# Kernel tuning notes

Hardware: AMD Instinct MI355X
Metric: run time of the kernel (lower is better)

Reference implementation:

```python
import jax, jax.numpy as jnp
import numpy as np

B, LQ, LK, DQ, DK, DV, H = 8, 256, 1024, 512, 512, 512, 128
NEG = -1000000.0

def setup_inputs() -> dict:
    key = jax.random.key(0)
    kq, kk, kv, kl, kwq, kwk, kwv = jax.random.split(key, 7)
    return {
        "Q": jax.random.normal(kq, (B, LQ, DQ), dtype=jnp.float32),
        "K": jax.random.normal(kk, (B, LK, DK), dtype=jnp.float32),
        "V": jax.random.normal(kv, (B, LK, DV), dtype=jnp.float32),
        "valid_lengths": jax.random.randint(kl, (B,), 1, LK + 1),
        "W_q": jax.random.normal(kwq, (DQ, H), dtype=jnp.float32) / np.sqrt(DQ),
        "W_k": jax.random.normal(kwk, (DK, H), dtype=jnp.float32) / np.sqrt(DK),
        "w_v": jax.random.normal(kwv, (H,), dtype=jnp.float32) / np.sqrt(H),
    }

def reference(Q, K, V, valid_lengths, W_q, W_k, w_v):
    # Projections
    q = Q @ W_q                      # (B, LQ, H)
    k = K @ W_k                      # (B, LK, H)
    # Additive (Bahdanau) features: broadcast add + tanh
    feat = jnp.tanh(q[:, :, None, :] + k[:, None, :, :])  # (B, LQ, LK, H)
    scores = jnp.einsum('bqkh,h->bqk', feat, w_v)          # (B, LQ, LK)
    # Masked softmax over keys (valid_lengths broadcast over all queries)
    mask = jnp.arange(LK)[None, None, :] < valid_lengths[:, None, None]
    scores = jnp.where(mask, scores, NEG)
    attn = jax.nn.softmax(scores, axis=-1)                 # (B, LQ, LK)
    # dropout_rate = 0.0 -> identity
    return jnp.einsum('bqk,bkd->bqd', attn, V)             # (B, LQ, DV)
```

## Files before the change

kernel.cpp:

```cpp
#include <hip/hip_runtime.h>

#define NBATCH 8
#define NLQ    256
#define NLK    1024
#define NDQ    512
#define NDV    512
#define NH     128
#define NEGV   -1000000.0f
#define TANH_SCALE 2.8853900817779268f
#define LOG2E      1.4426950408889634f

using f16x8 = __attribute__((ext_vector_type(8))) _Float16;
using f16x4 = __attribute__((ext_vector_type(4))) _Float16;
using f16x2 = __attribute__((ext_vector_type(2))) _Float16;
using f32x4 = __attribute__((ext_vector_type(4))) float;

__device__ __forceinline__ float fast_exp2(float x) {
#if __has_builtin(__builtin_amdgcn_exp2f)
  return __builtin_amdgcn_exp2f(x);
#else
  return exp2f(x);
#endif
}
__device__ __forceinline__ float fast_rcp(float x) {
#if __has_builtin(__builtin_amdgcn_rcpf)
  return __builtin_amdgcn_rcpf(x);
#else
  return 1.0f / x;
#endif
}

__global__ __launch_bounds__(256)
void prep_wT_kernel(const float* __restrict__ Wq, const float* __restrict__ Wk,
                    _Float16* __restrict__ wT) {
  const int idx = blockIdx.x * 256 + threadIdx.x;
  const int n = idx & 127;
  const int k = (idx >> 7) & 511;
  const int s = idx >> 16;
  const float* W = s ? Wk : Wq;
  wT[((size_t)(s * NH + n)) * NDQ + k] = (_Float16)W[k * NH + n];
}

__global__ __launch_bounds__(256)
void proj_mfma_kernel(const float* __restrict__ Q, const float* __restrict__ Kin,
                      const _Float16* __restrict__ wT, const int* __restrict__ vlen,
                      float* __restrict__ qp, float* __restrict__ ekT) {
  const int bx = blockIdx.x;
  const int nq = blockIdx.y;
  const bool isQ = (bx < 32);
  const float* A = isQ ? Q : Kin;
  const int m0 = (isQ ? bx : bx - 32) * 64;
  const int sIdx = isQ ? 0 : 1;

  if (!isQ) {
    const int b = m0 >> 10;
    if ((m0 & 1023) >= vlen[b]) return;
  }

  const int w = threadIdx.x >> 6, lane = threadIdx.x & 63;
  const int mrow = m0 + w * 16 + (lane & 15);
  const int kseg = (lane >> 4) * 8;

  const float* aBase = A + (size_t)mrow * NDQ + kseg;
  const _Float16* wt0 = wT + ((size_t)(sIdx * NH + nq * 32 +      (lane & 15))) * NDQ + kseg;
  const _Float16* wt1 = wT + ((size_t)(sIdx * NH + nq * 32 + 16 + (lane & 15))) * NDQ + kseg;

  f32x4 acc0 = {}, acc1 = {};
#pragma unroll 4
  for (int k0 = 0; k0 < NDQ; k0 += 32) {
    const float4 a0 = *(const float4*)&aBase[k0];
    const float4 a1 = *(const float4*)&aBase[k0 + 4];
    f16x8 af;
    af[0] = (_Float16)a0.x; af[1] = (_Float16)a0.y;
    af[2] = (_Float16)a0.z; af[3] = (_Float16)a0.w;
    af[4] = (_Float16)a1.x; af[5] = (_Float16)a1.y;
    af[6] = (_Float16)a1.z; af[7] = (_Float16)a1.w;
    const f16x8 b0 = *(const f16x8*)&wt0[k0];
    const f16x8 b1 = *(const f16x8*)&wt1[k0];
    acc0 = __builtin_amdgcn_mfma_f32_16x16x32_f16(af, b0, acc0, 0, 0, 0);
    acc1 = __builtin_amdgcn_mfma_f32_16x16x32_f16(af, b1, acc1, 0, 0, 0);
  }

  const int orow = m0 + w * 16 + (lane >> 4) * 4;
  const int col0 = nq * 32 + (lane & 15);
  if (isQ) {
#pragma unroll
    for (int r = 0; r < 4; ++r) {
      qp[(size_t)(orow + r) * NH + col0]      = fast_exp2(acc0[r] * TANH_SCALE);
      qp[(size_t)(orow + r) * NH + col0 + 16] = fast_exp2(acc1[r] * TANH_SCALE);
    }
  } else {
#pragma unroll
    for (int r = 0; r < 4; ++r) {
      const int grow = orow + r;
      const int b = grow >> 10, key = grow & 1023;
      ekT[((size_t)(b * NH) + col0)      * NLK + key] = fast_exp2(acc0[r] * TANH_SCALE);
      ekT[((size_t)(b * NH) + col0 + 16) * NLK + key] = fast_exp2(acc1[r] * TANH_SCALE);
    }
  }
}

__global__ __launch_bounds__(512)
void scores_softmax_kernel(const float* __restrict__ qp, const float* __restrict__ ekT,
                           const float* __restrict__ wv, const int* __restrict__ vlen,
                           _Float16* __restrict__ attnH) {
  const int qg = blockIdx.x;
  const int b  = blockIdx.y;
  const int w = threadIdx.x >> 6;
  const int lane = threadIdx.x & 63;
  const int key0 = w * 128 + lane * 2;

  __shared__ float redm[8][4];
  __shared__ float reds[8][4];

  const float* kcol  = &ekT[(size_t)b * NH * NLK + key0];
  const float* qbase = &qp[(size_t)(b * NLQ + qg * 4) * NH];
  const int VL = vlen[b];

  float2 acc[4] = {};
  if (w * 128 < VL) {
#pragma unroll 8
    for (int g = 0; g < 32; ++g) {
      const float4 w4 = *(const float4*)&wv[g * 4];
      float4 q4[4];
#pragma unroll
      for (int qi = 0; qi < 4; ++qi)
        q4[qi] = *(const float4*)&qbase[qi * NH + g * 4];
#pragma unroll
      for (int hh = 0; hh < 4; ++hh) {
        const float2 kv = *(const float2*)&kcol[(size_t)(g * 4 + hh) * NLK];
        const float wl = (hh == 0) ? w4.x : (hh == 1) ? w4.y : (hh == 2) ? w4.z : w4.w;
#pragma unroll
        for (int qi = 0; qi < 4; ++qi) {
          const float qs = (hh == 0) ? q4[qi].x : (hh == 1) ? q4[qi].y
                         : (hh == 2) ? q4[qi].z : q4[qi].w;
          acc[qi].x = fmaf(wl, fast_rcp(fmaf(qs, kv.x, 1.0f)), acc[qi].x);
          acc[qi].y = fmaf(wl, fast_rcp(fmaf(qs, kv.y, 1.0f)), acc[qi].y);
        }
      }
    }
  }

  float2 s[4];
#pragma unroll
  for (int qi = 0; qi < 4; ++qi) {
    s[qi].x = (key0 + 0 < VL) ? -2.0f * acc[qi].x : NEGV;
    s[qi].y = (key0 + 1 < VL) ? -2.0f * acc[qi].y : NEGV;
  }

#pragma unroll
  for (int qi = 0; qi < 4; ++qi) {
    float m = fmaxf(s[qi].x, s[qi].y);
#pragma unroll
    for (int off = 32; off > 0; off >>= 1) m = fmaxf(m, __shfl_xor(m, off));
    if (lane == 0) redm[w][qi] = m;
  }
  __syncthreads();
  float mg[4];
#pragma unroll
  for (int qi = 0; qi < 4; ++qi) {
    float m = redm[0][qi];
#pragma unroll
    for (int ww = 1; ww < 8; ++ww) m = fmaxf(m, redm[ww][qi]);
    mg[qi] = m;
  }

  float2 p[4];
#pragma unroll
  for (int qi = 0; qi < 4; ++qi) {
    p[qi].x = fast_exp2((s[qi].x - mg[qi]) * LOG2E);
    p[qi].y = fast_exp2((s[qi].y - mg[qi]) * LOG2E);
    float sum = p[qi].x + p[qi].y;
#pragma unroll
    for (int off = 32; off > 0; off >>= 1) sum += __shfl_xor(sum, off);
    if (lane == 0) reds[w][qi] = sum;
  }
  __syncthreads();

#pragma unroll
  for (int qi = 0; qi < 4; ++qi) {
    float tot = reds[0][qi];
#pragma unroll
    for (int ww = 1; ww < 8; ++ww) tot += reds[ww][qi];
    const float inv = fast_rcp(tot);
    f16x2 h;
    h[0] = (_Float16)(p[qi].x * inv);
    h[1] = (_Float16)(p[qi].y * inv);
    *(f16x2*)&attnH[(size_t)(b * NLQ + qg * 4 + qi) * NLK + key0] = h;
  }
}

__global__ __launch_bounds__(256)
void pv_mfma_kernel(const _Float16* __restrict__ attnH, const float* __restrict__ V,
                    const int* __restrict__ vlen, float* __restrict__ out) {
  const int b  = blockIdx.z;
  const int m0 = blockIdx.x * 64;
  const int n0 = blockIdx.y * 32;
  const int tid = threadIdx.x;
  const int w = tid >> 6, lane = tid & 63;
  const int kmax = (vlen[b] + 31) & ~31;

  __shared__ _Float16 aT[64][40];
  __shared__ _Float16 vT[32][32];

  const _Float16* aBase = attnH + (size_t)(b * NLQ + m0) * NLK;
  const float*    vBase = V + (size_t)b * NLK * NDV + n0;
  float*          oBase = out + (size_t)(b * NLQ + m0) * NDV + n0;

  const int ar = tid >> 2;
  const int ak = (tid & 3) * 8;
  const int vk = tid >> 3;
  const int vn = (tid & 7) * 4;
  const int vswz = ((vn >> 2) & 3) << 3;

  const int am  = w * 16 + (lane & 15);
  const int akf = (lane >> 4) * 8;
  const int bn  = lane & 15;
  const int bks = akf ^ (((bn >> 2) & 3) << 3);

  f32x4 acc0 = {}, acc1 = {};

  f16x8 aReg = *(const f16x8*)&aBase[(size_t)ar * NLK + ak];
  float4 vReg = *(const float4*)&vBase[(size_t)vk * NDV + vn];

  for (int k0 = 0; k0 < kmax; k0 += 32) {
    __syncthreads();
    *(f16x8*)&aT[ar][ak] = aReg;
    {
      const int ks = vk ^ vswz;
      vT[vn + 0][ks] = (_Float16)vReg.x;
      vT[vn + 1][ks] = (_Float16)vReg.y;
      vT[vn + 2][ks] = (_Float16)vReg.z;
      vT[vn + 3][ks] = (_Float16)vReg.w;
    }
    __syncthreads();

    if (k0 + 32 < kmax) {
      aReg = *(const f16x8*)&aBase[(size_t)ar * NLK + k0 + 32 + ak];
      vReg = *(const float4*)&vBase[(size_t)(k0 + 32 + vk) * NDV + vn];
    }

    const f16x8 af = *(const f16x8*)&aT[am][akf];
    const f16x8 bf0 = *(const f16x8*)&vT[ 0 + bn][bks];
    const f16x8 bf1 = *(const f16x8*)&vT[16 + bn][bks];
    acc0 = __builtin_amdgcn_mfma_f32_16x16x32_f16(af, bf0, acc0, 0, 0, 0);
    acc1 = __builtin_amdgcn_mfma_f32_16x16x32_f16(af, bf1, acc1, 0, 0, 0);
  }

  const int orow = w * 16 + (lane >> 4) * 4;
  const int ocol = lane & 15;
#pragma unroll
  for (int r = 0; r < 4; ++r) {
    oBase[(size_t)(orow + r) * NDV + ocol +  0] = acc0[r];
    oBase[(size_t)(orow + r) * NDV + ocol + 16] = acc1[r];
  }
}

extern "C" void kernel_launch(void* const* d_in, const int* in_sizes, int n_in,
                              void* d_out, int out_size, void* d_ws, size_t ws_size,
                              hipStream_t stream) {
  const float* Q    = (const float*)d_in[0];
  const float* Kin  = (const float*)d_in[1];
  const float* V    = (const float*)d_in[2];
  const int*   vlen = (const int*)d_in[3];
  const float* Wq   = (const float*)d_in[4];
  const float* Wk   = (const float*)d_in[5];
  const float* wv   = (const float*)d_in[6];
  float* out = (float*)d_out;

  float* qp  = (float*)d_ws;
  float* ekT = qp + NBATCH * NLQ * NH;
  _Float16* attnH = (_Float16*)(ekT + NBATCH * NH * NLK);
  _Float16* wT = attnH + (size_t)NBATCH * NLQ * NLK;

  hipLaunchKernelGGL(prep_wT_kernel, dim3(2 * NDQ * NH / 256), dim3(256), 0, stream,
                     Wq, Wk, wT);
  hipLaunchKernelGGL(proj_mfma_kernel, dim3(160, 4), dim3(256), 0, stream,
                     Q, Kin, wT, vlen, qp, ekT);
  hipLaunchKernelGGL(scores_softmax_kernel, dim3(64, NBATCH), dim3(512), 0, stream,
                     qp, ekT, wv, vlen, attnH);
  hipLaunchKernelGGL(pv_mfma_kernel, dim3(NLQ / 64, NDV / 32, NBATCH), dim3(256), 0, stream,
                     attnH, V, vlen, out);
}
```

Baseline: 75.27 us.

## Interleave projected keys by 4 heads and use one key per thread

The key projection output moves from a head-major transposed layout to a chunked layout where each key holds 4 consecutive heads contiguously. The scores kernel can then load a float4 per key per head group. Each thread now handles one key instead of two, and blocks grow to 1024 threads. The projection kernel computes 64 heads per block instead of 32, which halves the grid in y and reuses the A loads across more MFMAs. The trade-off is less reuse of the q loads per key load in the scores kernel, plus strided 4-byte scattered stores in the projection.

```diff
diff --git a/kernel.cpp b/kernel.cpp
--- a/kernel.cpp
+++ b/kernel.cpp
@@ -44,9 +44,9 @@
 __global__ __launch_bounds__(256)
 void proj_mfma_kernel(const float* __restrict__ Q, const float* __restrict__ Kin,
                       const _Float16* __restrict__ wT, const int* __restrict__ vlen,
-                      float* __restrict__ qp, float* __restrict__ ekT) {
+                      float* __restrict__ qp, float* __restrict__ ekC) {
   const int bx = blockIdx.x;
-  const int nq = blockIdx.y;
+  const int nh2 = blockIdx.y;
   const bool isQ = (bx < 32);
   const float* A = isQ ? Q : Kin;
   const int m0 = (isQ ? bx : bx - 32) * 64;
@@ -62,10 +62,9 @@
   const int kseg = (lane >> 4) * 8;
 
   const float* aBase = A + (size_t)mrow * NDQ + kseg;
-  const _Float16* wt0 = wT + ((size_t)(sIdx * NH + nq * 32 +      (lane & 15))) * NDQ + kseg;
-  const _Float16* wt1 = wT + ((size_t)(sIdx * NH + nq * 32 + 16 + (lane & 15))) * NDQ + kseg;
-
-  f32x4 acc0 = {}, acc1 = {};
+  const _Float16* wtb = wT + ((size_t)(sIdx * NH + nh2 * 64 + (lane & 15))) * NDQ + kseg;
+
+  f32x4 acc0 = {}, acc1 = {}, acc2 = {}, acc3 = {};
 #pragma unroll 4
   for (int k0 = 0; k0 < NDQ; k0 += 32) {
     const float4 a0 = *(const float4*)&aBase[k0];
@@ -75,82 +74,88 @@
     af[2] = (_Float16)a0.z; af[3] = (_Float16)a0.w;
     af[4] = (_Float16)a1.x; af[5] = (_Float16)a1.y;
     af[6] = (_Float16)a1.z; af[7] = (_Float16)a1.w;
-    const f16x8 b0 = *(const f16x8*)&wt0[k0];
-    const f16x8 b1 = *(const f16x8*)&wt1[k0];
+    const f16x8 b0 = *(const f16x8*)&wtb[k0];
+    const f16x8 b1 = *(const f16x8*)&wtb[(size_t)16 * NDQ + k0];
+    const f16x8 b2 = *(const f16x8*)&wtb[(size_t)32 * NDQ + k0];
+    const f16x8 b3 = *(const f16x8*)&wtb[(size_t)48 * NDQ + k0];
     acc0 = __builtin_amdgcn_mfma_f32_16x16x32_f16(af, b0, acc0, 0, 0, 0);
     acc1 = __builtin_amdgcn_mfma_f32_16x16x32_f16(af, b1, acc1, 0, 0, 0);
+    acc2 = __builtin_amdgcn_mfma_f32_16x16x32_f16(af, b2, acc2, 0, 0, 0);
+    acc3 = __builtin_amdgcn_mfma_f32_16x16x32_f16(af, b3, acc3, 0, 0, 0);
   }
 
   const int orow = m0 + w * 16 + (lane >> 4) * 4;
-  const int col0 = nq * 32 + (lane & 15);
+  const int col0 = nh2 * 64 + (lane & 15);
   if (isQ) {
 #pragma unroll
     for (int r = 0; r < 4; ++r) {
       qp[(size_t)(orow + r) * NH + col0]      = fast_exp2(acc0[r] * TANH_SCALE);
       qp[(size_t)(orow + r) * NH + col0 + 16] = fast_exp2(acc1[r] * TANH_SCALE);
+      qp[(size_t)(orow + r) * NH + col0 + 32] = fast_exp2(acc2[r] * TANH_SCALE);
+      qp[(size_t)(orow + r) * NH + col0 + 48] = fast_exp2(acc3[r] * TANH_SCALE);
     }
   } else {
 #pragma unroll
     for (int r = 0; r < 4; ++r) {
       const int grow = orow + r;
       const int b = grow >> 10, key = grow & 1023;
-      ekT[((size_t)(b * NH) + col0)      * NLK + key] = fast_exp2(acc0[r] * TANH_SCALE);
-      ekT[((size_t)(b * NH) + col0 + 16) * NLK + key] = fast_exp2(acc1[r] * TANH_SCALE);
-    }
-  }
-}
-
-__global__ __launch_bounds__(512)
-void scores_softmax_kernel(const float* __restrict__ qp, const float* __restrict__ ekT,
+      const float v0 = fast_exp2(acc0[r] * TANH_SCALE);
+      const float v1 = fast_exp2(acc1[r] * TANH_SCALE);
+      const float v2 = fast_exp2(acc2[r] * TANH_SCALE);
+      const float v3 = fast_exp2(acc3[r] * TANH_SCALE);
+      const int c0 = col0, c1 = col0 + 16, c2 = col0 + 32, c3 = col0 + 48;
+      ekC[(((size_t)b * 32 + (c0 >> 2)) * NLK + key) * 4 + (c0 & 3)] = v0;
+      ekC[(((size_t)b * 32 + (c1 >> 2)) * NLK + key) * 4 + (c1 & 3)] = v1;
+      ekC[(((size_t)b * 32 + (c2 >> 2)) * NLK + key) * 4 + (c2 & 3)] = v2;
+      ekC[(((size_t)b * 32 + (c3 >> 2)) * NLK + key) * 4 + (c3 & 3)] = v3;
+    }
+  }
+}
+
+__global__ __launch_bounds__(1024)
+void scores_softmax_kernel(const float* __restrict__ qp, const float* __restrict__ ekC,
                            const float* __restrict__ wv, const int* __restrict__ vlen,
                            _Float16* __restrict__ attnH) {
   const int qg = blockIdx.x;
   const int b  = blockIdx.y;
   const int w = threadIdx.x >> 6;
   const int lane = threadIdx.x & 63;
-  const int key0 = w * 128 + lane * 2;
-
-  __shared__ float redm[8][4];
-  __shared__ float reds[8][4];
-
-  const float* kcol  = &ekT[(size_t)b * NH * NLK + key0];
+  const int key = w * 64 + lane;
+
+  __shared__ float redm[16][4];
+  __shared__ float reds[16][4];
+
+  const float* kbase = &ekC[(((size_t)b * 32) * NLK + key) * 4];
   const float* qbase = &qp[(size_t)(b * NLQ + qg * 4) * NH];
   const int VL = vlen[b];
 
-  float2 acc[4] = {};
-  if (w * 128 < VL) {
+  float acc[4] = {};
+  if (w * 64 < VL) {
 #pragma unroll 8
     for (int g = 0; g < 32; ++g) {
+      const float4 kv = *(const float4*)&kbase[(size_t)g * NLK * 4];
       const float4 w4 = *(const float4*)&wv[g * 4];
-      float4 q4[4];
-#pragma unroll
-      for (int qi = 0; qi < 4; ++qi)
-        q4[qi] = *(const float4*)&qbase[qi * NH + g * 4];
-#pragma unroll
-      for (int hh = 0; hh < 4; ++hh) {
-        const float2 kv = *(const float2*)&kcol[(size_t)(g * 4 + hh) * NLK];
-        const float wl = (hh == 0) ? w4.x : (hh == 1) ? w4.y : (hh == 2) ? w4.z : w4.w;
-#pragma unroll
-        for (int qi = 0; qi < 4; ++qi) {
-          const float qs = (hh == 0) ? q4[qi].x : (hh == 1) ? q4[qi].y
-                         : (hh == 2) ? q4[qi].z : q4[qi].w;
-          acc[qi].x = fmaf(wl, fast_rcp(fmaf(qs, kv.x, 1.0f)), acc[qi].x);
-          acc[qi].y = fmaf(wl, fast_rcp(fmaf(qs, kv.y, 1.0f)), acc[qi].y);
-        }
+#pragma unroll
+      for (int qi = 0; qi < 4; ++qi) {
+        const float4 q4 = *(const float4*)&qbase[qi * NH + g * 4];
+        float a = acc[qi];
+        a = fmaf(w4.x, fast_rcp(fmaf(q4.x, kv.x, 1.0f)), a);
+        a = fmaf(w4.y, fast_rcp(fmaf(q4.y, kv.y, 1.0f)), a);
+        a = fmaf(w4.z, fast_rcp(fmaf(q4.z, kv.z, 1.0f)), a);
+        a = fmaf(w4.w, fast_rcp(fmaf(q4.w, kv.w, 1.0f)), a);
+        acc[qi] = a;
       }
     }
   }
 
-  float2 s[4];
-#pragma unroll
-  for (int qi = 0; qi < 4; ++qi) {
-    s[qi].x = (key0 + 0 < VL) ? -2.0f * acc[qi].x : NEGV;
-    s[qi].y = (key0 + 1 < VL) ? -2.0f * acc[qi].y : NEGV;
-  }
-
-#pragma unroll
-  for (int qi = 0; qi < 4; ++qi) {
-    float m = fmaxf(s[qi].x, s[qi].y);
+  float s[4];
+#pragma unroll
+  for (int qi = 0; qi < 4; ++qi)
+    s[qi] = (key < VL) ? -2.0f * acc[qi] : NEGV;
+
+#pragma unroll
+  for (int qi = 0; qi < 4; ++qi) {
+    float m = s[qi];
 #pragma unroll
     for (int off = 32; off > 0; off >>= 1) m = fmaxf(m, __shfl_xor(m, off));
     if (lane == 0) redm[w][qi] = m;
@@ -161,16 +166,15 @@
   for (int qi = 0; qi < 4; ++qi) {
     float m = redm[0][qi];
 #pragma unroll
-    for (int ww = 1; ww < 8; ++ww) m = fmaxf(m, redm[ww][qi]);
+    for (int ww = 1; ww < 16; ++ww) m = fmaxf(m, redm[ww][qi]);
     mg[qi] = m;
   }
 
-  float2 p[4];
-#pragma unroll
-  for (int qi = 0; qi < 4; ++qi) {
-    p[qi].x = fast_exp2((s[qi].x - mg[qi]) * LOG2E);
-    p[qi].y = fast_exp2((s[qi].y - mg[qi]) * LOG2E);
-    float sum = p[qi].x + p[qi].y;
+  float p[4];
+#pragma unroll
+  for (int qi = 0; qi < 4; ++qi) {
+    p[qi] = fast_exp2((s[qi] - mg[qi]) * LOG2E);
+    float sum = p[qi];
 #pragma unroll
     for (int off = 32; off > 0; off >>= 1) sum += __shfl_xor(sum, off);
     if (lane == 0) reds[w][qi] = sum;
@@ -181,12 +185,9 @@
   for (int qi = 0; qi < 4; ++qi) {
     float tot = reds[0][qi];
 #pragma unroll
-    for (int ww = 1; ww < 8; ++ww) tot += reds[ww][qi];
+    for (int ww = 1; ww < 16; ++ww) tot += reds[ww][qi];
     const float inv = fast_rcp(tot);
-    f16x2 h;
-    h[0] = (_Float16)(p[qi].x * inv);
-    h[1] = (_Float16)(p[qi].y * inv);
-    *(f16x2*)&attnH[(size_t)(b * NLQ + qg * 4 + qi) * NLK + key0] = h;
+    attnH[(size_t)(b * NLQ + qg * 4 + qi) * NLK + key] = (_Float16)(p[qi] * inv);
   }
 }
 
@@ -269,16 +270,16 @@
   float* out = (float*)d_out;
 
   float* qp  = (float*)d_ws;
-  float* ekT = qp + NBATCH * NLQ * NH;
-  _Float16* attnH = (_Float16*)(ekT + NBATCH * NH * NLK);
+  float* ekC = qp + NBATCH * NLQ * NH;
+  _Float16* attnH = (_Float16*)(ekC + NBATCH * NH * NLK);
   _Float16* wT = attnH + (size_t)NBATCH * NLQ * NLK;
 
   hipLaunchKernelGGL(prep_wT_kernel, dim3(2 * NDQ * NH / 256), dim3(256), 0, stream,
                      Wq, Wk, wT);
-  hipLaunchKernelGGL(proj_mfma_kernel, dim3(160, 4), dim3(256), 0, stream,
-                     Q, Kin, wT, vlen, qp, ekT);
-  hipLaunchKernelGGL(scores_softmax_kernel, dim3(64, NBATCH), dim3(512), 0, stream,
-                     qp, ekT, wv, vlen, attnH);
+  hipLaunchKernelGGL(proj_mfma_kernel, dim3(160, 2), dim3(256), 0, stream,
+                     Q, Kin, wT, vlen, qp, ekC);
+  hipLaunchKernelGGL(scores_softmax_kernel, dim3(64, NBATCH), dim3(1024), 0, stream,
+                     qp, ekC, wv, vlen, attnH);
   hipLaunchKernelGGL(pv_mfma_kernel, dim3(NLQ / 64, NDV / 32, NBATCH), dim3(256), 0, stream,
                      attnH, V, vlen, out);
 }
```

New measurement: 88.95 us. 1.18x slower.

## Store exp-projected keys as fp16 pairs and software-pipeline key loads

Applied to the files above, without the earlier changes.

The projected key exponentials (ekT) are now stored in fp16, with pairs of hidden channels interleaved per key, so each thread gets two keys by two channels in one 8-byte load. The scores loop is manually unrolled by two groups and double-buffers those key loads to hide latency. This halves the key-feature traffic and load count in the tanh/score inner loop. In exchange it loses precision on exp(2k) values, whose range in fp16 may saturate for large projections, and the register use of the scores kernel goes up.

```diff
diff --git a/kernel.cpp b/kernel.cpp
--- a/kernel.cpp
+++ b/kernel.cpp
@@ -44,7 +44,7 @@
 __global__ __launch_bounds__(256)
 void proj_mfma_kernel(const float* __restrict__ Q, const float* __restrict__ Kin,
                       const _Float16* __restrict__ wT, const int* __restrict__ vlen,
-                      float* __restrict__ qp, float* __restrict__ ekT) {
+                      float* __restrict__ qp, _Float16* __restrict__ ekTp) {
   const int bx = blockIdx.x;
   const int nq = blockIdx.y;
   const bool isQ = (bx < 32);
@@ -94,14 +94,17 @@
     for (int r = 0; r < 4; ++r) {
       const int grow = orow + r;
       const int b = grow >> 10, key = grow & 1023;
-      ekT[((size_t)(b * NH) + col0)      * NLK + key] = fast_exp2(acc0[r] * TANH_SCALE);
-      ekT[((size_t)(b * NH) + col0 + 16) * NLK + key] = fast_exp2(acc1[r] * TANH_SCALE);
+      const int c0 = col0, c1 = col0 + 16;
+      ekTp[(((size_t)b * 64 + (c0 >> 1)) * NLK + key) * 2 + (c0 & 1)] =
+          (_Float16)fast_exp2(acc0[r] * TANH_SCALE);
+      ekTp[(((size_t)b * 64 + (c1 >> 1)) * NLK + key) * 2 + (c1 & 1)] =
+          (_Float16)fast_exp2(acc1[r] * TANH_SCALE);
     }
   }
 }
 
 __global__ __launch_bounds__(512)
-void scores_softmax_kernel(const float* __restrict__ qp, const float* __restrict__ ekT,
+void scores_softmax_kernel(const float* __restrict__ qp, const _Float16* __restrict__ ekTp,
                            const float* __restrict__ wv, const int* __restrict__ vlen,
                            _Float16* __restrict__ attnH) {
   const int qg = blockIdx.x;
@@ -113,29 +116,73 @@
   __shared__ float redm[8][4];
   __shared__ float reds[8][4];
 
-  const float* kcol  = &ekT[(size_t)b * NH * NLK + key0];
+  const _Float16* kcol = ekTp + ((size_t)b * 64 * NLK + key0) * 2;
   const float* qbase = &qp[(size_t)(b * NLQ + qg * 4) * NH];
   const int VL = vlen[b];
 
   float2 acc[4] = {};
   if (w * 128 < VL) {
-#pragma unroll 8
-    for (int g = 0; g < 32; ++g) {
-      const float4 w4 = *(const float4*)&wv[g * 4];
-      float4 q4[4];
-#pragma unroll
-      for (int qi = 0; qi < 4; ++qi)
-        q4[qi] = *(const float4*)&qbase[qi * NH + g * 4];
-#pragma unroll
-      for (int hh = 0; hh < 4; ++hh) {
-        const float2 kv = *(const float2*)&kcol[(size_t)(g * 4 + hh) * NLK];
-        const float wl = (hh == 0) ? w4.x : (hh == 1) ? w4.y : (hh == 2) ? w4.z : w4.w;
+    f16x4 pA0, pA1, pB0, pB1;
+    pA0 = *(const f16x4*)&kcol[(size_t)0 * NLK * 2];
+    pA1 = *(const f16x4*)&kcol[(size_t)1 * NLK * 2];
+
+#pragma unroll
+    for (int g = 0; g < 32; g += 2) {
+      pB0 = *(const f16x4*)&kcol[(size_t)(2 * g + 2) * NLK * 2];
+      pB1 = *(const f16x4*)&kcol[(size_t)(2 * g + 3) * NLK * 2];
+
+      {
+        const float4 w4 = *(const float4*)&wv[g * 4];
+        float4 q4[4];
+#pragma unroll
+        for (int qi = 0; qi < 4; ++qi)
+          q4[qi] = *(const float4*)&qbase[qi * NH + g * 4];
+        const float kx0 = (float)pA0[0], ky0 = (float)pA0[2];
+        const float kx1 = (float)pA0[1], ky1 = (float)pA0[3];
+        const float kx2 = (float)pA1[0], ky2 = (float)pA1[2];
+        const float kx3 = (float)pA1[1], ky3 = (float)pA1[3];
 #pragma unroll
         for (int qi = 0; qi < 4; ++qi) {
-          const float qs = (hh == 0) ? q4[qi].x : (hh == 1) ? q4[qi].y
-                         : (hh == 2) ? q4[qi].z : q4[qi].w;
-          acc[qi].x = fmaf(wl, fast_rcp(fmaf(qs, kv.x, 1.0f)), acc[qi].x);
-          acc[qi].y = fmaf(wl, fast_rcp(fmaf(qs, kv.y, 1.0f)), acc[qi].y);
+          float ax = acc[qi].x, ay = acc[qi].y;
+          ax = fmaf(w4.x, fast_rcp(fmaf(q4[qi].x, kx0, 1.0f)), ax);
+          ay = fmaf(w4.x, fast_rcp(fmaf(q4[qi].x, ky0, 1.0f)), ay);
+          ax = fmaf(w4.y, fast_rcp(fmaf(q4[qi].y, kx1, 1.0f)), ax);
+          ay = fmaf(w4.y, fast_rcp(fmaf(q4[qi].y, ky1, 1.0f)), ay);
+          ax = fmaf(w4.z, fast_rcp(fmaf(q4[qi].z, kx2, 1.0f)), ax);
+          ay = fmaf(w4.z, fast_rcp(fmaf(q4[qi].z, ky2, 1.0f)), ay);
+          ax = fmaf(w4.w, fast_rcp(fmaf(q4[qi].w, kx3, 1.0f)), ax);
+          ay = fmaf(w4.w, fast_rcp(fmaf(q4[qi].w, ky3, 1.0f)), ay);
+          acc[qi].x = ax; acc[qi].y = ay;
+        }
+      }
+
+      if (g + 2 < 32) {
+        pA0 = *(const f16x4*)&kcol[(size_t)(2 * g + 4) * NLK * 2];
+        pA1 = *(const f16x4*)&kcol[(size_t)(2 * g + 5) * NLK * 2];
+      }
+
+      {
+        const float4 w4 = *(const float4*)&wv[(g + 1) * 4];
+        float4 q4[4];
+#pragma unroll
+        for (int qi = 0; qi < 4; ++qi)
+          q4[qi] = *(const float4*)&qbase[qi * NH + (g + 1) * 4];
+        const float kx0 = (float)pB0[0], ky0 = (float)pB0[2];
+        const float kx1 = (float)pB0[1], ky1 = (float)pB0[3];
+        const float kx2 = (float)pB1[0], ky2 = (float)pB1[2];
+        const float kx3 = (float)pB1[1], ky3 = (float)pB1[3];
+#pragma unroll
+        for (int qi = 0; qi < 4; ++qi) {
+          float ax = acc[qi].x, ay = acc[qi].y;
+          ax = fmaf(w4.x, fast_rcp(fmaf(q4[qi].x, kx0, 1.0f)), ax);
+          ay = fmaf(w4.x, fast_rcp(fmaf(q4[qi].x, ky0, 1.0f)), ay);
+          ax = fmaf(w4.y, fast_rcp(fmaf(q4[qi].y, kx1, 1.0f)), ax);
+          ay = fmaf(w4.y, fast_rcp(fmaf(q4[qi].y, ky1, 1.0f)), ay);
+          ax = fmaf(w4.z, fast_rcp(fmaf(q4[qi].z, kx2, 1.0f)), ax);
+          ay = fmaf(w4.z, fast_rcp(fmaf(q4[qi].z, ky2, 1.0f)), ay);
+          ax = fmaf(w4.w, fast_rcp(fmaf(q4[qi].w, kx3, 1.0f)), ax);
+          ay = fmaf(w4.w, fast_rcp(fmaf(q4[qi].w, ky3, 1.0f)), ay);
+          acc[qi].x = ax; acc[qi].y = ay;
         }
       }
     }
@@ -268,17 +315,17 @@
   const float* wv   = (const float*)d_in[6];
   float* out = (float*)d_out;
 
-  float* qp  = (float*)d_ws;
-  float* ekT = qp + NBATCH * NLQ * NH;
-  _Float16* attnH = (_Float16*)(ekT + NBATCH * NH * NLK);
+  float* qp = (float*)d_ws;
+  _Float16* ekTp = (_Float16*)(qp + NBATCH * NLQ * NH);
+  _Float16* attnH = ekTp + (size_t)NBATCH * NH * NLK;
   _Float16* wT = attnH + (size_t)NBATCH * NLQ * NLK;
 
   hipLaunchKernelGGL(prep_wT_kernel, dim3(2 * NDQ * NH / 256), dim3(256), 0, stream,
                      Wq, Wk, wT);
   hipLaunchKernelGGL(proj_mfma_kernel, dim3(160, 4), dim3(256), 0, stream,
-                     Q, Kin, wT, vlen, qp, ekT);
+                     Q, Kin, wT, vlen, qp, ekTp);
   hipLaunchKernelGGL(scores_softmax_kernel, dim3(64, NBATCH), dim3(512), 0, stream,
-                     qp, ekT, wv, vlen, attnH);
+                     qp, ekTp, wv, vlen, attnH);
   hipLaunchKernelGGL(pv_mfma_kernel, dim3(NLQ / 64, NDV / 32, NBATCH), dim3(256), 0, stream,
                      attnH, V, vlen, out);
 }
```

Result: no change. 74.83 us (-0.6%).
